# Performance work log

Measured on AMD Instinct MI355X. Metric: run time of the kernel, lower is better.

Reference implementation:

```python
import jax, jax.numpy as jnp
import numpy as np

LEAKY = 0.5      # args.leaky
TEMP = 1.0       # args.temp
N_USER = 100000  # args.user
N_ITEM = 50000   # args.item
LATDIM = 128     # args.latdim
HYPERNUM = 128   # args.hyperNum
N_LAYERS = 2     # args.gnn_layer
N_EDGES = 1000000
BATCH = 4096


def _leaky(x):
    return jnp.maximum(LEAKY * x, x)


def _l2norm(x):
    # torch.nn.functional.normalize(p=2, dim=1): x / max(||x||, 1e-12)
    n = jnp.linalg.norm(x, axis=1, keepdims=True)
    return x / jnp.maximum(n, 1e-12)


def _spmm(rows, cols, vals, x, n_out):
    # torch.sparse.mm(adj, x) with adj given as COO (rows, cols, vals)
    return jax.ops.segment_sum(vals[:, None] * x[cols], rows, num_segments=n_out)


def _hyper_prop(lats, adj, Ws):
    # lats: [N, D], adj: [N, H] (dense hyper adjacency), Ws: [3, H, H]
    lat = _leaky(adj.T @ lats)                    # [H, D]
    for k in range(3):
        # (LeakyRelu(lat.T @ W)).T + lat == LeakyRelu(W.T @ lat) + lat
        lat = _leaky(Ws[k].T @ lat) + lat
    return _leaky(adj @ lat)                      # [N, D]


def _ssl(hyperLat, gnnLat):
    pos = jnp.exp(jnp.sum(hyperLat * gnnLat, axis=1) / TEMP)
    neg = jnp.sum(jnp.exp(gnnLat @ hyperLat.T / TEMP), axis=1)
    return jnp.sum(-jnp.log(pos / (neg + 1e-8) + 1e-8))


def setup_inputs() -> dict:
    key = jax.random.key(0)
    ks = jax.random.split(key, 12)
    # distinct ids so jnp.sort(ids) == torch.unique(ids)
    uids = jax.random.permutation(ks[0], N_USER)[:BATCH].astype(jnp.int32)
    iids = jax.random.permutation(ks[1], N_ITEM)[:BATCH].astype(jnp.int32)
    adj_rows = jax.random.randint(ks[2], (N_EDGES,), 0, N_USER, dtype=jnp.int32)
    adj_cols = jax.random.randint(ks[3], (N_EDGES,), 0, N_ITEM, dtype=jnp.int32)
    adj_vals = jax.random.uniform(ks[4], (N_EDGES,), dtype=jnp.float32)
    s_emb = 0.05
    s_hh = (2.0 / (HYPERNUM + HYPERNUM)) ** 0.5   # xavier_normal
    s_dh = (2.0 / (LATDIM + HYPERNUM)) ** 0.5
    s_dd = (2.0 / (LATDIM + LATDIM)) ** 0.5
    uEmbed0 = jax.random.normal(ks[5], (N_USER, LATDIM), jnp.float32) * s_emb
    iEmbed0 = jax.random.normal(ks[6], (N_ITEM, LATDIM), jnp.float32) * s_emb
    uhyper = jax.random.normal(ks[7], (LATDIM, HYPERNUM), jnp.float32) * s_dh
    ihyper = jax.random.normal(ks[8], (LATDIM, HYPERNUM), jnp.float32) * s_dh
    Wu = jax.random.normal(ks[9], (N_LAYERS, 3, HYPERNUM, HYPERNUM), jnp.float32) * s_hh
    Wi = jax.random.normal(ks[10], (N_LAYERS, 3, HYPERNUM, HYPERNUM), jnp.float32) * s_hh
    Wt = jax.random.normal(ks[11], (N_LAYERS, LATDIM, LATDIM), jnp.float32) * s_dd
    return {"uids": uids, "iids": iids, "adj_rows": adj_rows, "adj_cols": adj_cols,
            "adj_vals": adj_vals, "uEmbed0": uEmbed0, "iEmbed0": iEmbed0,
            "uhyper": uhyper, "ihyper": ihyper, "Wu": Wu, "Wi": Wi, "Wt": Wt}


def reference(uids, iids, adj_rows, adj_cols, adj_vals, uEmbed0, iEmbed0,
              uhyper, ihyper, Wu, Wi, Wt):
    # droprate = 0 => edgeDropout and feature dropout are identity
    uuHyper = uEmbed0 @ uhyper   # [N_USER, H]
    iiHyper = iEmbed0 @ ihyper   # [N_ITEM, H]
    ulats, ilats = [uEmbed0], [iEmbed0]
    gnnU, gnnI, hypU, hypI = [], [], [], []
    for l in range(N_LAYERS):
        ulat = _leaky(_spmm(adj_rows, adj_cols, adj_vals, ilats[-1], N_USER))
        ilat = _leaky(_spmm(adj_cols, adj_rows, adj_vals, ulats[-1], N_ITEM))
        hu = _hyper_prop(ulats[-1], uuHyper, Wu[l])
        hi = _hyper_prop(ilats[-1], iiHyper, Wi[l])
        gnnU.append(ulat); gnnI.append(ilat); hypU.append(hu); hypI.append(hi)
        ulats.append(ulat + hu + ulats[-1])
        ilats.append(ilat + hi + ilats[-1])
    ulat = sum(ulats)
    ilat = sum(ilats)
    preds = jnp.sum(ulat[uids] * ilat[iids], axis=-1)
    uniqU = jnp.sort(uids)  # uids are distinct -> equals torch.unique
    uniqI = jnp.sort(iids)
    ssl = jnp.asarray(0.0, jnp.float32)
    for l in range(N_LAYERS):
        ssl = ssl + _ssl(_l2norm(hypU[l][uniqU]) @ Wt[l], _l2norm(gnnU[l][uniqU]))
        ssl = ssl + _ssl(_l2norm(hypI[l][uniqI]) @ Wt[l], _l2norm(gnnI[l][uniqI]))
    reg = (jnp.sum(jnp.square(uEmbed0)) + jnp.sum(jnp.square(iEmbed0)) +
           jnp.sum(jnp.square(uhyper)) + jnp.sum(jnp.square(ihyper)))
    return preds, ssl, reg
```

## Files before the change

kernel.cpp:

```cpp
#include <hip/hip_runtime.h>

#define NU 100000
#define NI 50000
#define DD 128
#define HH 128
#define NE 1000000
#define NB 4096
#define SCHUNK 2048
#define ATBB 512

__device__ __forceinline__ float lk(float x) { return fmaxf(0.5f * x, x); }

__global__ __launch_bounds__(256) void hist_kernel(const int* __restrict__ idx,
                                                   int* __restrict__ deg, int n) {
  int e = blockIdx.x * 256 + threadIdx.x;
  if (e < n) atomicAdd(&deg[idx[e]], 1);
}

__global__ __launch_bounds__(256) void scan_bsum(const int* __restrict__ deg,
                                                 int* __restrict__ bsum, int N) {
  int b = blockIdx.x, t = threadIdx.x;
  int base = b * SCHUNK;
  int s = 0;
  for (int i = t; i < SCHUNK; i += 256) {
    int g = base + i;
    if (g < N) s += deg[g];
  }
#pragma unroll
  for (int o = 32; o > 0; o >>= 1) s += __shfl_down(s, o);
  __shared__ int ws[4];
  if ((t & 63) == 0) ws[t >> 6] = s;
  __syncthreads();
  if (t == 0) bsum[b] = ws[0] + ws[1] + ws[2] + ws[3];
}

__global__ __launch_bounds__(256) void scan_top(int* __restrict__ bsum, int G) {
  int t = threadIdx.x;
  __shared__ int sh[256];
  int v = (t < G) ? bsum[t] : 0;
  sh[t] = v;
  __syncthreads();
  for (int o = 1; o < 256; o <<= 1) {
    int add = (t >= o) ? sh[t - o] : 0;
    __syncthreads();
    sh[t] += add;
    __syncthreads();
  }
  if (t < G) bsum[t] = sh[t] - v;
}

__global__ __launch_bounds__(256) void scan_write(const int* __restrict__ deg,
                                                  const int* __restrict__ bsumx,
                                                  int* __restrict__ rowptr,
                                                  int* __restrict__ cursor,
                                                  int N, int total) {
  int b = blockIdx.x, t = threadIdx.x;
  int base = b * SCHUNK + t * 8;
  int v[8], s = 0;
#pragma unroll
  for (int i = 0; i < 8; i++) {
    int g = base + i;
    v[i] = (g < N) ? deg[g] : 0;
    s += v[i];
  }
  __shared__ int sh[256];
  sh[t] = s;
  __syncthreads();
  for (int o = 1; o < 256; o <<= 1) {
    int add = (t >= o) ? sh[t - o] : 0;
    __syncthreads();
    sh[t] += add;
    __syncthreads();
  }
  int off = bsumx[b] + sh[t] - s;
#pragma unroll
  for (int i = 0; i < 8; i++) {
    int g = base + i;
    if (g < N) { rowptr[g] = off; cursor[g] = off; }
    off += v[i];
  }
  if (b == 0 && t == 0) rowptr[N] = total;
}

__global__ __launch_bounds__(256) void scatter_kernel(const int* __restrict__ idx,
                                                      const int* __restrict__ other,
                                                      const float* __restrict__ vals,
                                                      int* __restrict__ cursor,
                                                      int* __restrict__ scol,
                                                      float* __restrict__ sval, int n) {
  int e = blockIdx.x * 256 + threadIdx.x;
  if (e < n) {
    int p = atomicAdd(&cursor[idx[e]], 1);
    scol[p] = other[e];
    sval[p] = vals[e];
  }
}

__global__ __launch_bounds__(256) void spmm_csr_kernel(
    const int* __restrict__ rowptr, const int* __restrict__ scol,
    const float* __restrict__ sval, const float* __restrict__ x,
    float* __restrict__ y, int N) {
  int w = (blockIdx.x * 256 + threadIdx.x) >> 6;
  if (w >= N) return;
  int lane = threadIdx.x & 63;
  int half = lane >> 5, l32 = lane & 31;
  const float4* x4 = (const float4*)x;
  int j0 = rowptr[w], j1 = rowptr[w + 1];
  float ax = 0.f, ay = 0.f, az = 0.f, aw = 0.f;
  int j = j0 + half;
  for (; j + 2 < j1; j += 4) {
    int c0 = scol[j], c1 = scol[j + 2];
    float v0 = sval[j], v1 = sval[j + 2];
    float4 x0 = x4[(size_t)c0 * 32 + l32];
    float4 x1 = x4[(size_t)c1 * 32 + l32];
    ax += v0 * x0.x + v1 * x1.x;
    ay += v0 * x0.y + v1 * x1.y;
    az += v0 * x0.z + v1 * x1.z;
    aw += v0 * x0.w + v1 * x1.w;
  }
  for (; j < j1; j += 2) {
    int c0 = scol[j];
    float v0 = sval[j];
    float4 x0 = x4[(size_t)c0 * 32 + l32];
    ax += v0 * x0.x; ay += v0 * x0.y; az += v0 * x0.z; aw += v0 * x0.w;
  }
  ax += __shfl_xor(ax, 32); ay += __shfl_xor(ay, 32);
  az += __shfl_xor(az, 32); aw += __shfl_xor(aw, 32);
  if (half == 0) {
    float4 r; r.x = ax; r.y = ay; r.z = az; r.w = aw;
    ((float4*)y)[(size_t)w * 32 + l32] = r;
  }
}

__global__ __launch_bounds__(256) void atb_kernel(
    const float* __restrict__ E, const float* __restrict__ X,
    float* __restrict__ part, int N) {
  __shared__ __align__(16) float Es[64][132];
  __shared__ __align__(16) float Xs[64][132];
  int t = threadIdx.x;
  int ip = (t >> 4) << 2;
  int jp = (t & 15) << 2;
  int rpb = (N + (int)gridDim.x - 1) / (int)gridDim.x;
  int n0 = blockIdx.x * rpb;
  int n1 = min(n0 + rpb, N);
  float acc[2][2][4][4] = {};
  const float4* E4 = (const float4*)E;
  const float4* X4 = (const float4*)X;
  for (int n = n0; n < n1; n += 64) {
    int nr = min(64, n1 - n);
    __syncthreads();
#pragma unroll
    for (int q = 0; q < 8; q++) {
      int f = t + (q << 8);
      int row = f >> 5, c4 = f & 31;
      float4 ev = {0.f, 0.f, 0.f, 0.f}, xv = {0.f, 0.f, 0.f, 0.f};
      if (row < nr) {
        size_t gi = (size_t)(n + row) * 32 + c4;
        ev = E4[gi]; xv = X4[gi];
      }
      *(float4*)&Es[row][c4 << 2] = ev;
      *(float4*)&Xs[row][c4 << 2] = xv;
    }
    __syncthreads();
#pragma unroll 2
    for (int rr = 0; rr < 64; rr++) {
      float4 e0 = *(const float4*)&Es[rr][ip];
      float4 e1 = *(const float4*)&Es[rr][ip + 64];
      float4 x0 = *(const float4*)&Xs[rr][jp];
      float4 x1 = *(const float4*)&Xs[rr][jp + 64];
      const float* e0p = (const float*)&e0;
      const float* e1p = (const float*)&e1;
      const float* x0p = (const float*)&x0;
      const float* x1p = (const float*)&x1;
#pragma unroll
      for (int ai = 0; ai < 4; ai++)
#pragma unroll
        for (int aj = 0; aj < 4; aj++) {
          acc[0][0][ai][aj] += e0p[ai] * x0p[aj];
          acc[0][1][ai][aj] += e0p[ai] * x1p[aj];
          acc[1][0][ai][aj] += e1p[ai] * x0p[aj];
          acc[1][1][ai][aj] += e1p[ai] * x1p[aj];
        }
    }
  }
  float* dst = part + (size_t)blockIdx.x * 16384;
#pragma unroll
  for (int rh = 0; rh < 2; rh++)
#pragma unroll
    for (int ai = 0; ai < 4; ai++) {
      int row = rh * 64 + ip + ai;
#pragma unroll
      for (int ch = 0; ch < 2; ch++) {
        float4 v;
        v.x = acc[rh][ch][ai][0]; v.y = acc[rh][ch][ai][1];
        v.z = acc[rh][ch][ai][2]; v.w = acc[rh][ch][ai][3];
        *(float4*)&dst[row * 128 + ch * 64 + jp] = v;
      }
    }
}

__global__ __launch_bounds__(256) void reduce_atb_kernel(
    const float* __restrict__ part, float* __restrict__ A) {
  int e4 = blockIdx.x * 256 + threadIdx.x;
  const float4* p4 = (const float4*)part;
  float4 s = {0.f, 0.f, 0.f, 0.f};
#pragma unroll 4
  for (int b = 0; b < ATBB; b++) {
    float4 v = p4[(size_t)b * 4096 + e4];
    s.x += v.x; s.y += v.y; s.z += v.z; s.w += v.w;
  }
  ((float4*)A)[e4] = s;
}

__global__ __launch_bounds__(256) void chain_kernel(
    const float* __restrict__ A_u, const float* __restrict__ A_i,
    const float* __restrict__ uhy, const float* __restrict__ ihy,
    const float* __restrict__ Wu_l, const float* __restrict__ Wi_l,
    float* __restrict__ B_u, float* __restrict__ B_i) {
  __shared__ float Wb[128 * 132];
  __shared__ float LA[128][16];
  __shared__ float LB[128][16];
  int side = blockIdx.x >> 3, strip = blockIdx.x & 7;
  const float* A = side ? A_i : A_u;
  const float* hy = side ? ihy : uhy;
  const float* W = side ? Wi_l : Wu_l;
  float* Bo = side ? B_i : B_u;
  int t = threadIdx.x;
  int j0 = strip * 16;
  for (int i = t; i < 2048; i += 256) LA[i >> 4][i & 15] = A[(i >> 4) * 128 + j0 + (i & 15)];
  for (int i = t; i < 16384; i += 256) Wb[(i >> 7) * 132 + (i & 127)] = hy[i];
  __syncthreads();
  int jc = t & 15, i0 = (t >> 4) * 8;
  {
    float acc[8] = {};
    for (int k = 0; k < 128; k++) {
      float lv = LA[k][jc];
      const float* wr = &Wb[k * 132 + i0];
#pragma unroll
      for (int a = 0; a < 8; a++) acc[a] += wr[a] * lv;
    }
#pragma unroll
    for (int a = 0; a < 8; a++) LB[i0 + a][jc] = lk(acc[a]);
  }
  __syncthreads();
  float (*pin)[16] = LB;
  float (*pout)[16] = LA;
  for (int s = 0; s < 3; s++) {
    for (int i = t; i < 16384; i += 256) Wb[(i >> 7) * 132 + (i & 127)] = W[s * 16384 + i];
    __syncthreads();
    float acc[8] = {};
    for (int k = 0; k < 128; k++) {
      float lv = pin[k][jc];
      const float* wr = &Wb[k * 132 + i0];
#pragma unroll
      for (int a = 0; a < 8; a++) acc[a] += wr[a] * lv;
    }
#pragma unroll
    for (int a = 0; a < 8; a++) pout[i0 + a][jc] = lk(acc[a]) + pin[i0 + a][jc];
    __syncthreads();
    float (*tmp)[16] = pin; pin = pout; pout = tmp;
  }
  for (int i = t; i < 16384; i += 256) Wb[(i >> 7) * 132 + (i & 127)] = hy[i];
  __syncthreads();
  {
    int i = t >> 1, jb = (t & 1) * 8;
    float acc[8] = {};
    for (int k = 0; k < 128; k++) {
      float hv = Wb[i * 132 + k];
      const float* lr = &pin[k][jb];
#pragma unroll
      for (int b = 0; b < 8; b++) acc[b] += hv * lr[b];
    }
#pragma unroll
    for (int b = 0; b < 8; b++) Bo[i * 128 + j0 + jb + b] = acc[b];
  }
}

__global__ __launch_bounds__(256) void nmul_upd_kernel(
    const float* __restrict__ E, const float* __restrict__ Bm,
    const float* __restrict__ gnn, float* __restrict__ cur, int N) {
  __shared__ __align__(16) float Bs[128][132];
  __shared__ __align__(16) float Es[128][132];
  int t = threadIdx.x;
  int rg = t >> 4, dg = t & 15;
  for (int k = t; k < 16384; k += 256) Bs[k >> 7][k & 127] = Bm[k];
  int ntiles = (N + 127) >> 7;
  for (int tile = blockIdx.x; tile < ntiles; tile += gridDim.x) {
    int n0 = tile << 7;
    int nr = min(128, N - n0);
    __syncthreads();
    for (int k = t; k < 16384; k += 256) {
      int rr = k >> 7, cc = k & 127;
      Es[rr][cc] = (rr < nr) ? E[(size_t)(n0 + rr) * DD + cc] : 0.f;
    }
    __syncthreads();
    float acc[8][8] = {};
    for (int h4 = 0; h4 < 128; h4 += 4) {
      float4 ev[8];
#pragma unroll
      for (int a = 0; a < 8; a++) ev[a] = *(const float4*)&Es[rg + (a << 4)][h4];
#pragma unroll
      for (int hh = 0; hh < 4; hh++) {
        float4 b0 = *(const float4*)&Bs[h4 + hh][dg << 2];
        float4 b1 = *(const float4*)&Bs[h4 + hh][(dg << 2) + 64];
#pragma unroll
        for (int a = 0; a < 8; a++) {
          float e = ((const float*)&ev[a])[hh];
          acc[a][0] += e * b0.x; acc[a][1] += e * b0.y;
          acc[a][2] += e * b0.z; acc[a][3] += e * b0.w;
          acc[a][4] += e * b1.x; acc[a][5] += e * b1.y;
          acc[a][6] += e * b1.z; acc[a][7] += e * b1.w;
        }
      }
    }
#pragma unroll
    for (int a = 0; a < 8; a++) {
      int n = n0 + rg + (a << 4);
      if (n < N) {
        size_t base = (size_t)n * DD + (dg << 2);
        float4 g0 = *(const float4*)(gnn + base);
        float4 g1 = *(const float4*)(gnn + base + 64);
        float4 c0 = *(const float4*)(cur + base);
        float4 c1 = *(const float4*)(cur + base + 64);
        c0.x += lk(g0.x) + lk(acc[a][0]); c0.y += lk(g0.y) + lk(acc[a][1]);
        c0.z += lk(g0.z) + lk(acc[a][2]); c0.w += lk(g0.w) + lk(acc[a][3]);
        c1.x += lk(g1.x) + lk(acc[a][4]); c1.y += lk(g1.y) + lk(acc[a][5]);
        c1.z += lk(g1.z) + lk(acc[a][6]); c1.w += lk(g1.w) + lk(acc[a][7]);
        *(float4*)(cur + base) = c0; *(float4*)(cur + base + 64) = c1;
      }
    }
  }
}

__global__ __launch_bounds__(128) void sslgath_kernel(
    const int* __restrict__ ids, const float* __restrict__ gnn,
    const float* __restrict__ E, const float* __restrict__ Bm,
    float* __restrict__ og, float* __restrict__ oh) {
  __shared__ __align__(16) float Bs[128][132];
  __shared__ __align__(16) float Eb[32][132];
  __shared__ int idb[32];
  int t = threadIdx.x;
  int base = blockIdx.x * 32;
  if (t < 32) idb[t] = ids[base + t];
#pragma unroll
  for (int q = 0; q < 32; q++) {
    int f = t + q * 128;
    *(float4*)&Bs[f >> 5][(f & 31) << 2] = ((const float4*)Bm)[f];
  }
  __syncthreads();
#pragma unroll
  for (int q = 0; q < 8; q++) {
    int f = t + q * 128;
    int r = f >> 5, c4 = f & 31;
    *(float4*)&Eb[r][c4 << 2] = ((const float4*)E)[(size_t)idb[r] * 32 + c4];
  }
  __syncthreads();
  float acc[32] = {};
  for (int k = 0; k < 128; k++) {
    float b = Bs[k][t];
#pragma unroll
    for (int r = 0; r < 32; r++) acc[r] += Eb[r][k] * b;
  }
  for (int r = 0; r < 32; r++) {
    int id = idb[r];
    og[(size_t)(base + r) * DD + t] = lk(gnn[(size_t)id * DD + t]);
    oh[(size_t)(base + r) * DD + t] = lk(acc[r]);
  }
}

__global__ __launch_bounds__(128) void gaccum_kernel(
    const int* __restrict__ ids, const float* __restrict__ cur,
    float* __restrict__ sumg) {
  int b = blockIdx.x, d = threadIdx.x;
  int id = ids[b];
  sumg[(size_t)b * DD + d] += cur[(size_t)id * DD + d];
}

__global__ __launch_bounds__(256) void preds_kernel(
    const float* __restrict__ su, const float* __restrict__ si,
    float* __restrict__ outp) {
  int gid = blockIdx.x * 256 + threadIdx.x;
  int w = gid >> 6, lane = gid & 63;
  if (w >= NB) return;
  float2 a = *(const float2*)(su + (size_t)w * DD + 2 * lane);
  float2 b = *(const float2*)(si + (size_t)w * DD + 2 * lane);
  float d = a.x * b.x + a.y * b.y;
#pragma unroll
  for (int o = 32; o > 0; o >>= 1) d += __shfl_down(d, o);
  if (lane == 0) outp[w] = d;
}

__global__ __launch_bounds__(256) void sumsq_kernel(
    const float* __restrict__ x, int n, float* __restrict__ outp) {
  float acc = 0.f;
  for (int i = blockIdx.x * 256 + threadIdx.x; i < n; i += gridDim.x * 256) {
    float v = x[i];
    acc += v * v;
  }
#pragma unroll
  for (int o = 32; o > 0; o >>= 1) acc += __shfl_down(acc, o);
  __shared__ float s[4];
  if ((threadIdx.x & 63) == 0) s[threadIdx.x >> 6] = acc;
  __syncthreads();
  if (threadIdx.x == 0) atomicAdd(outp, s[0] + s[1] + s[2] + s[3]);
}

__global__ __launch_bounds__(128) void norm_kernel(
    const float* __restrict__ gh, float* __restrict__ gg,
    float* __restrict__ hn) {
  int r = blockIdx.x, d = threadIdx.x;
  __shared__ float red[4];
  float hv = gh[(size_t)r * DD + d];
  float gv = gg[(size_t)r * DD + d];
  float h2 = hv * hv, g2 = gv * gv;
#pragma unroll
  for (int o = 32; o > 0; o >>= 1) { h2 += __shfl_down(h2, o); g2 += __shfl_down(g2, o); }
  if ((d & 63) == 0) { red[(d >> 6) * 2] = h2; red[(d >> 6) * 2 + 1] = g2; }
  __syncthreads();
  float hnorm = sqrtf(red[0] + red[2]);
  float gnorm = sqrtf(red[1] + red[3]);
  hn[(size_t)r * DD + d] = hv / fmaxf(hnorm, 1e-12f);
  gg[(size_t)r * DD + d] = gv / fmaxf(gnorm, 1e-12f);
}

__global__ __launch_bounds__(256) void nmul_plain_kernel(
    const float* __restrict__ In, const float* __restrict__ Wm,
    float* __restrict__ outp) {
  __shared__ __align__(16) float Bs[128][132];
  __shared__ __align__(16) float Es[128][132];
  int t = threadIdx.x;
  int rg = t >> 4, dg = t & 15;
  int n0 = blockIdx.x << 7;
  for (int k = t; k < 16384; k += 256) {
    Bs[k >> 7][k & 127] = Wm[k];
    Es[k >> 7][k & 127] = In[(size_t)n0 * DD + k];
  }
  __syncthreads();
  float acc[8][8] = {};
  for (int h4 = 0; h4 < 128; h4 += 4) {
    float4 ev[8];
#pragma unroll
    for (int a = 0; a < 8; a++) ev[a] = *(const float4*)&Es[rg + (a << 4)][h4];
#pragma unroll
    for (int hh = 0; hh < 4; hh++) {
      float4 b0 = *(const float4*)&Bs[h4 + hh][dg << 2];
      float4 b1 = *(const float4*)&Bs[h4 + hh][(dg << 2) + 64];
#pragma unroll
      for (int a = 0; a < 8; a++) {
        float e = ((const float*)&ev[a])[hh];
        acc[a][0] += e * b0.x; acc[a][1] += e * b0.y;
        acc[a][2] += e * b0.z; acc[a][3] += e * b0.w;
        acc[a][4] += e * b1.x; acc[a][5] += e * b1.y;
        acc[a][6] += e * b1.z; acc[a][7] += e * b1.w;
      }
    }
  }
#pragma unroll
  for (int a = 0; a < 8; a++) {
    size_t base = (size_t)(n0 + rg + (a << 4)) * DD + (dg << 2);
    float4 v0, v1;
    v0.x = acc[a][0]; v0.y = acc[a][1]; v0.z = acc[a][2]; v0.w = acc[a][3];
    v1.x = acc[a][4]; v1.y = acc[a][5]; v1.z = acc[a][6]; v1.w = acc[a][7];
    *(float4*)(outp + base) = v0;
    *(float4*)(outp + base + 64) = v1;
  }
}

__global__ __launch_bounds__(256) void gram_kernel(
    const float* __restrict__ gn, const float* __restrict__ hw,
    float* __restrict__ neg) {
  __shared__ __align__(16) float Gs[128][132];
  __shared__ __align__(16) float Ht[128][132];
  int t = threadIdx.x;
  int rg = t >> 4, jp = (t & 15) << 2;
  int i0 = blockIdx.x << 7, j0 = blockIdx.y << 7;
  for (int k = t; k < 16384; k += 256) {
    int rr = k >> 7, cc = k & 127;
    Gs[rr][cc] = gn[(size_t)(i0 + rr) * DD + cc];
    Ht[cc][rr] = hw[(size_t)(j0 + rr) * DD + cc];
  }
  __syncthreads();
  float acc[8][8] = {};
  for (int h4 = 0; h4 < 128; h4 += 4) {
    float4 ev[8];
#pragma unroll
    for (int a = 0; a < 8; a++) ev[a] = *(const float4*)&Gs[rg + (a << 4)][h4];
#pragma unroll
    for (int hh = 0; hh < 4; hh++) {
      float4 b0 = *(const float4*)&Ht[h4 + hh][jp];
      float4 b1 = *(const float4*)&Ht[h4 + hh][jp + 64];
#pragma unroll
      for (int a = 0; a < 8; a++) {
        float g = ((const float*)&ev[a])[hh];
        acc[a][0] += g * b0.x; acc[a][1] += g * b0.y;
        acc[a][2] += g * b0.z; acc[a][3] += g * b0.w;
        acc[a][4] += g * b1.x; acc[a][5] += g * b1.y;
        acc[a][6] += g * b1.z; acc[a][7] += g * b1.w;
      }
    }
  }
#pragma unroll
  for (int a = 0; a < 8; a++) {
    float s = 0.f;
#pragma unroll
    for (int b = 0; b < 8; b++) s += expf(acc[a][b]);
    s += __shfl_xor(s, 1);
    s += __shfl_xor(s, 2);
    s += __shfl_xor(s, 4);
    s += __shfl_xor(s, 8);
    if ((t & 15) == 0) atomicAdd(&neg[i0 + rg + (a << 4)], s);
  }
}

__global__ __launch_bounds__(256) void sslfin_kernel(
    const float* __restrict__ gn, const float* __restrict__ hw,
    const float* __restrict__ neg, float* __restrict__ outp) {
  int gid = blockIdx.x * 256 + threadIdx.x;
  int w = gid >> 6, lane = gid & 63;
  if (w >= NB) return;
  float2 a = *(const float2*)(gn + (size_t)w * DD + 2 * lane);
  float2 b = *(const float2*)(hw + (size_t)w * DD + 2 * lane);
  float d = a.x * b.x + a.y * b.y;
#pragma unroll
  for (int o = 32; o > 0; o >>= 1) d += __shfl_down(d, o);
  if (lane == 0) {
    float pos = expf(d);
    float v = -logf(pos / (neg[w] + 1e-8f) + 1e-8f);
    atomicAdd(outp, v);
  }
}

extern "C" void kernel_launch(void* const* d_in, const int* in_sizes, int n_in,
                              void* d_out, int out_size, void* d_ws, size_t ws_size,
                              hipStream_t stream) {
  (void)in_sizes; (void)n_in; (void)out_size; (void)ws_size;
  const int* uids = (const int*)d_in[0];
  const int* iids = (const int*)d_in[1];
  const int* arow = (const int*)d_in[2];
  const int* acol = (const int*)d_in[3];
  const float* avals = (const float*)d_in[4];
  const float* uE = (const float*)d_in[5];
  const float* iE = (const float*)d_in[6];
  const float* uhy = (const float*)d_in[7];
  const float* ihy = (const float*)d_in[8];
  const float* Wu = (const float*)d_in[9];
  const float* Wi = (const float*)d_in[10];
  const float* Wt = (const float*)d_in[11];
  float* out = (float*)d_out;

  float* p = (float*)d_ws;
  float* cur_u = p; p += (size_t)NU * DD;
  float* gnn_u = p; p += (size_t)NU * DD;
  float* cur_i = p; p += (size_t)NI * DD;
  float* gnn_i = p; p += (size_t)NI * DD;
  float* A_u = p; p += HH * DD;
  float* A_i = p; p += HH * DD;
  float* B_u = p; p += HH * DD;
  float* B_i = p; p += HH * DD;
  float* sumg_u = p; p += (size_t)NB * DD;
  float* sumg_i = p; p += (size_t)NB * DD;
  float* region = p; p += (size_t)ATBB * 16384;
  float* negb = p; p += 4 * NB;
  int* rowptr_u = (int*)p; p += NU + 1;
  int* cursor_u = (int*)p; p += NU;
  int* rowptr_i = (int*)p; p += NI + 1;
  int* cursor_i = (int*)p; p += NI;
  int* bsum = (int*)p; p += 256;
  int* scol_u = (int*)p; p += NE;
  float* sval_u = p; p += NE;
  int* scol_i = (int*)p; p += NE;
  float* sval_i = p; p += NE;

  float* Apart = region;
  float* gg = region;
  float* gh = region + (size_t)NB * DD;
  float* hn = region + 2 * (size_t)NB * DD;

  const int GU = (NU + SCHUNK - 1) / SCHUNK;
  const int GI = (NI + SCHUNK - 1) / SCHUNK;
  const int EB = (NE + 255) / 256;

  hipMemsetAsync(cursor_u, 0, NU * sizeof(int), stream);
  hist_kernel<<<EB, 256, 0, stream>>>(arow, cursor_u, NE);
  scan_bsum<<<GU, 256, 0, stream>>>(cursor_u, bsum, NU);
  scan_top<<<1, 256, 0, stream>>>(bsum, GU);
  scan_write<<<GU, 256, 0, stream>>>(cursor_u, bsum, rowptr_u, cursor_u, NU, NE);
  scatter_kernel<<<EB, 256, 0, stream>>>(arow, acol, avals, cursor_u, scol_u, sval_u, NE);

  hipMemsetAsync(cursor_i, 0, NI * sizeof(int), stream);
  hist_kernel<<<EB, 256, 0, stream>>>(acol, cursor_i, NE);
  scan_bsum<<<GI, 256, 0, stream>>>(cursor_i, bsum, NI);
  scan_top<<<1, 256, 0, stream>>>(bsum, GI);
  scan_write<<<GI, 256, 0, stream>>>(cursor_i, bsum, rowptr_i, cursor_i, NI, NE);
  scatter_kernel<<<EB, 256, 0, stream>>>(acol, arow, avals, cursor_i, scol_i, sval_i, NE);

  hipMemcpyAsync(cur_u, uE, (size_t)NU * DD * 4, hipMemcpyDeviceToDevice, stream);
  hipMemcpyAsync(cur_i, iE, (size_t)NI * DD * 4, hipMemcpyDeviceToDevice, stream);
  hipMemsetAsync(out + NB, 0, 2 * sizeof(float), stream);
  hipMemsetAsync(negb, 0, 4 * NB * sizeof(float), stream);
  hipMemsetAsync(sumg_u, 0, 2 * (size_t)NB * DD * 4, stream);
  gaccum_kernel<<<NB, 128, 0, stream>>>(uids, uE, sumg_u);
  gaccum_kernel<<<NB, 128, 0, stream>>>(iids, iE, sumg_i);

  for (int l = 0; l < 2; l++) {
    const float* Wt_l = Wt + (size_t)l * DD * DD;
    spmm_csr_kernel<<<NU / 4, 256, 0, stream>>>(rowptr_u, scol_u, sval_u, cur_i, gnn_u, NU);
    spmm_csr_kernel<<<NI / 4, 256, 0, stream>>>(rowptr_i, scol_i, sval_i, cur_u, gnn_i, NI);
    atb_kernel<<<ATBB, 256, 0, stream>>>(uE, cur_u, Apart, NU);
    reduce_atb_kernel<<<16, 256, 0, stream>>>(Apart, A_u);
    atb_kernel<<<ATBB, 256, 0, stream>>>(iE, cur_i, Apart, NI);
    reduce_atb_kernel<<<16, 256, 0, stream>>>(Apart, A_i);
    chain_kernel<<<16, 256, 0, stream>>>(A_u, A_i, uhy, ihy,
        Wu + (size_t)l * 3 * HH * HH, Wi + (size_t)l * 3 * HH * HH, B_u, B_i);

    sslgath_kernel<<<NB / 32, 128, 0, stream>>>(uids, gnn_u, uE, B_u, gg, gh);
    nmul_upd_kernel<<<512, 256, 0, stream>>>(uE, B_u, gnn_u, cur_u, NU);
    gaccum_kernel<<<NB, 128, 0, stream>>>(uids, cur_u, sumg_u);
    norm_kernel<<<NB, 128, 0, stream>>>(gh, gg, hn);
    nmul_plain_kernel<<<NB / 128, 256, 0, stream>>>(hn, Wt_l, gh);
    gram_kernel<<<dim3(NB / 128, NB / 128), 256, 0, stream>>>(gg, gh, negb + (2 * l) * NB);
    sslfin_kernel<<<NB / 4, 256, 0, stream>>>(gg, gh, negb + (2 * l) * NB, out + NB);

    sslgath_kernel<<<NB / 32, 128, 0, stream>>>(iids, gnn_i, iE, B_i, gg, gh);
    nmul_upd_kernel<<<512, 256, 0, stream>>>(iE, B_i, gnn_i, cur_i, NI);
    gaccum_kernel<<<NB, 128, 0, stream>>>(iids, cur_i, sumg_i);
    norm_kernel<<<NB, 128, 0, stream>>>(gh, gg, hn);
    nmul_plain_kernel<<<NB / 128, 256, 0, stream>>>(hn, Wt_l, gh);
    gram_kernel<<<dim3(NB / 128, NB / 128), 256, 0, stream>>>(gg, gh, negb + (2 * l + 1) * NB);
    sslfin_kernel<<<NB / 4, 256, 0, stream>>>(gg, gh, negb + (2 * l + 1) * NB, out + NB);
  }

  preds_kernel<<<NB / 4, 256, 0, stream>>>(sumg_u, sumg_i, out);
  sumsq_kernel<<<2048, 256, 0, stream>>>(uE, NU * DD, out + NB + 1);
  sumsq_kernel<<<1024, 256, 0, stream>>>(iE, NI * DD, out + NB + 1);
  sumsq_kernel<<<64, 256, 0, stream>>>(uhy, DD * HH, out + NB + 1);
  sumsq_kernel<<<64, 256, 0, stream>>>(ihy, DD * HH, out + NB + 1);
}
```

Measured before the change: 2.390 ms.

## Restructure dense GEMM kernels to stream activations from global and shrink LDS tiles

Three dense matmul kernels (node update, Wt projection, SSL gram) stop staging the activation tile in shared memory. Each thread now reads its rows straight from global memory as float4 and keeps only the 128x128 (or 64x128, XOR-swizzled) weight tile in LDS. Tiles are smaller and grids larger (one 128-row tile per block with 512 threads, 32-row blocks, 64-column gram tiles), which raises occupancy and parallelism for the small 4096-row SSL matrices. The cost is repeated global or L2 reads of activations across the thread groups that share a row, and lower register-level reuse per thread.

```diff
diff --git a/kernel.cpp b/kernel.cpp
--- a/kernel.cpp
+++ b/kernel.cpp
@@ -276,58 +276,59 @@
   }
 }
 
-__global__ __launch_bounds__(256) void nmul_upd_kernel(
+__global__ __launch_bounds__(512) void nmul_upd_kernel(
     const float* __restrict__ E, const float* __restrict__ Bm,
     const float* __restrict__ gnn, float* __restrict__ cur, int N) {
-  __shared__ __align__(16) float Bs[128][132];
-  __shared__ __align__(16) float Es[128][132];
+  __shared__ __align__(16) float Bs[128][128];
   int t = threadIdx.x;
-  int rg = t >> 4, dg = t & 15;
-  for (int k = t; k < 16384; k += 256) Bs[k >> 7][k & 127] = Bm[k];
-  int ntiles = (N + 127) >> 7;
-  for (int tile = blockIdx.x; tile < ntiles; tile += gridDim.x) {
-    int n0 = tile << 7;
-    int nr = min(128, N - n0);
-    __syncthreads();
-    for (int k = t; k < 16384; k += 256) {
-      int rr = k >> 7, cc = k & 127;
-      Es[rr][cc] = (rr < nr) ? E[(size_t)(n0 + rr) * DD + cc] : 0.f;
-    }
-    __syncthreads();
-    float acc[8][8] = {};
-    for (int h4 = 0; h4 < 128; h4 += 4) {
-      float4 ev[8];
-#pragma unroll
-      for (int a = 0; a < 8; a++) ev[a] = *(const float4*)&Es[rg + (a << 4)][h4];
-#pragma unroll
-      for (int hh = 0; hh < 4; hh++) {
-        float4 b0 = *(const float4*)&Bs[h4 + hh][dg << 2];
-        float4 b1 = *(const float4*)&Bs[h4 + hh][(dg << 2) + 64];
-#pragma unroll
-        for (int a = 0; a < 8; a++) {
-          float e = ((const float*)&ev[a])[hh];
-          acc[a][0] += e * b0.x; acc[a][1] += e * b0.y;
-          acc[a][2] += e * b0.z; acc[a][3] += e * b0.w;
-          acc[a][4] += e * b1.x; acc[a][5] += e * b1.y;
-          acc[a][6] += e * b1.z; acc[a][7] += e * b1.w;
-        }
+  int dg = t & 15, rg = t >> 4;
+  const float4* B4 = (const float4*)Bm;
+#pragma unroll
+  for (int q = 0; q < 8; q++) {
+    int f = t + (q << 9);
+    *(float4*)&Bs[f >> 5][(f & 31) << 2] = B4[f];
+  }
+  __syncthreads();
+  int n0 = blockIdx.x << 7;
+  const float4* E4 = (const float4*)E;
+  float acc[4][8] = {};
+  int rows[4];
+  bool val[4];
+#pragma unroll
+  for (int a = 0; a < 4; a++) { rows[a] = n0 + rg + (a << 5); val[a] = rows[a] < N; }
+  for (int h4 = 0; h4 < 128; h4 += 4) {
+    float4 ev[4];
+#pragma unroll
+    for (int a = 0; a < 4; a++)
+      ev[a] = val[a] ? E4[(size_t)rows[a] * 32 + (h4 >> 2)]
+                     : make_float4(0.f, 0.f, 0.f, 0.f);
+#pragma unroll
+    for (int hh = 0; hh < 4; hh++) {
+      float4 b0 = *(const float4*)&Bs[h4 + hh][dg << 2];
+      float4 b1 = *(const float4*)&Bs[h4 + hh][(dg << 2) + 64];
+#pragma unroll
+      for (int a = 0; a < 4; a++) {
+        float e = ((const float*)&ev[a])[hh];
+        acc[a][0] += e * b0.x; acc[a][1] += e * b0.y;
+        acc[a][2] += e * b0.z; acc[a][3] += e * b0.w;
+        acc[a][4] += e * b1.x; acc[a][5] += e * b1.y;
+        acc[a][6] += e * b1.z; acc[a][7] += e * b1.w;
       }
     }
-#pragma unroll
-    for (int a = 0; a < 8; a++) {
-      int n = n0 + rg + (a << 4);
-      if (n < N) {
-        size_t base = (size_t)n * DD + (dg << 2);
-        float4 g0 = *(const float4*)(gnn + base);
-        float4 g1 = *(const float4*)(gnn + base + 64);
-        float4 c0 = *(const float4*)(cur + base);
-        float4 c1 = *(const float4*)(cur + base + 64);
-        c0.x += lk(g0.x) + lk(acc[a][0]); c0.y += lk(g0.y) + lk(acc[a][1]);
-        c0.z += lk(g0.z) + lk(acc[a][2]); c0.w += lk(g0.w) + lk(acc[a][3]);
-        c1.x += lk(g1.x) + lk(acc[a][4]); c1.y += lk(g1.y) + lk(acc[a][5]);
-        c1.z += lk(g1.z) + lk(acc[a][6]); c1.w += lk(g1.w) + lk(acc[a][7]);
-        *(float4*)(cur + base) = c0; *(float4*)(cur + base + 64) = c1;
-      }
+  }
+#pragma unroll
+  for (int a = 0; a < 4; a++) {
+    if (val[a]) {
+      size_t base = (size_t)rows[a] * DD + (dg << 2);
+      float4 g0 = *(const float4*)(gnn + base);
+      float4 g1 = *(const float4*)(gnn + base + 64);
+      float4 c0 = *(const float4*)(cur + base);
+      float4 c1 = *(const float4*)(cur + base + 64);
+      c0.x += lk(g0.x) + lk(acc[a][0]); c0.y += lk(g0.y) + lk(acc[a][1]);
+      c0.z += lk(g0.z) + lk(acc[a][2]); c0.w += lk(g0.w) + lk(acc[a][3]);
+      c1.x += lk(g1.x) + lk(acc[a][4]); c1.y += lk(g1.y) + lk(acc[a][5]);
+      c1.z += lk(g1.z) + lk(acc[a][6]); c1.w += lk(g1.w) + lk(acc[a][7]);
+      *(float4*)(cur + base) = c0; *(float4*)(cur + base + 64) = c1;
     }
   }
 }
@@ -426,27 +427,30 @@
 __global__ __launch_bounds__(256) void nmul_plain_kernel(
     const float* __restrict__ In, const float* __restrict__ Wm,
     float* __restrict__ outp) {
-  __shared__ __align__(16) float Bs[128][132];
-  __shared__ __align__(16) float Es[128][132];
+  __shared__ __align__(16) float Bs[128][128];
   int t = threadIdx.x;
-  int rg = t >> 4, dg = t & 15;
-  int n0 = blockIdx.x << 7;
-  for (int k = t; k < 16384; k += 256) {
-    Bs[k >> 7][k & 127] = Wm[k];
-    Es[k >> 7][k & 127] = In[(size_t)n0 * DD + k];
-  }
-  __syncthreads();
-  float acc[8][8] = {};
+  int dg = t & 15, rg = t >> 4;
+  const float4* W4 = (const float4*)Wm;
+#pragma unroll
+  for (int q = 0; q < 16; q++) {
+    int f = t + (q << 8);
+    *(float4*)&Bs[f >> 5][(f & 31) << 2] = W4[f];
+  }
+  __syncthreads();
+  int n0 = blockIdx.x << 5;
+  const float4* I4 = (const float4*)In;
+  float acc[2][8] = {};
   for (int h4 = 0; h4 < 128; h4 += 4) {
-    float4 ev[8];
-#pragma unroll
-    for (int a = 0; a < 8; a++) ev[a] = *(const float4*)&Es[rg + (a << 4)][h4];
+    float4 ev[2];
+#pragma unroll
+    for (int a = 0; a < 2; a++)
+      ev[a] = I4[(size_t)(n0 + rg + (a << 4)) * 32 + (h4 >> 2)];
 #pragma unroll
     for (int hh = 0; hh < 4; hh++) {
       float4 b0 = *(const float4*)&Bs[h4 + hh][dg << 2];
       float4 b1 = *(const float4*)&Bs[h4 + hh][(dg << 2) + 64];
 #pragma unroll
-      for (int a = 0; a < 8; a++) {
+      for (int a = 0; a < 2; a++) {
         float e = ((const float*)&ev[a])[hh];
         acc[a][0] += e * b0.x; acc[a][1] += e * b0.y;
         acc[a][2] += e * b0.z; acc[a][3] += e * b0.w;
@@ -456,7 +460,7 @@
     }
   }
 #pragma unroll
-  for (int a = 0; a < 8; a++) {
+  for (int a = 0; a < 2; a++) {
     size_t base = (size_t)(n0 + rg + (a << 4)) * DD + (dg << 2);
     float4 v0, v1;
     v0.x = acc[a][0]; v0.y = acc[a][1]; v0.z = acc[a][2]; v0.w = acc[a][3];
@@ -469,46 +473,48 @@
 __global__ __launch_bounds__(256) void gram_kernel(
     const float* __restrict__ gn, const float* __restrict__ hw,
     float* __restrict__ neg) {
-  __shared__ __align__(16) float Gs[128][132];
-  __shared__ __align__(16) float Ht[128][132];
+  __shared__ __align__(16) float Hs[64][128];
   int t = threadIdx.x;
-  int rg = t >> 4, jp = (t & 15) << 2;
-  int i0 = blockIdx.x << 7, j0 = blockIdx.y << 7;
-  for (int k = t; k < 16384; k += 256) {
-    int rr = k >> 7, cc = k & 127;
-    Gs[rr][cc] = gn[(size_t)(i0 + rr) * DD + cc];
-    Ht[cc][rr] = hw[(size_t)(j0 + rr) * DD + cc];
-  }
-  __syncthreads();
-  float acc[8][8] = {};
+  int rg = t >> 4, dg = t & 15;
+  int i0 = blockIdx.x << 7, j0 = blockIdx.y << 6;
+  float4* Hs4 = (float4*)Hs;
+  const float4* hw4 = (const float4*)hw;
+#pragma unroll
+  for (int q = 0; q < 8; q++) {
+    int f = t + (q << 8);
+    int j = f >> 5, k4 = f & 31;
+    Hs4[j * 32 + (k4 ^ ((j >> 2) & 7))] = hw4[(size_t)(j0 + j) * 32 + k4];
+  }
+  __syncthreads();
+  const float4* G4 = (const float4*)gn;
+  float acc[8][4] = {};
   for (int h4 = 0; h4 < 128; h4 += 4) {
-    float4 ev[8];
-#pragma unroll
-    for (int a = 0; a < 8; a++) ev[a] = *(const float4*)&Gs[rg + (a << 4)][h4];
-#pragma unroll
-    for (int hh = 0; hh < 4; hh++) {
-      float4 b0 = *(const float4*)&Ht[h4 + hh][jp];
-      float4 b1 = *(const float4*)&Ht[h4 + hh][jp + 64];
-#pragma unroll
-      for (int a = 0; a < 8; a++) {
-        float g = ((const float*)&ev[a])[hh];
-        acc[a][0] += g * b0.x; acc[a][1] += g * b0.y;
-        acc[a][2] += g * b0.z; acc[a][3] += g * b0.w;
-        acc[a][4] += g * b1.x; acc[a][5] += g * b1.y;
-        acc[a][6] += g * b1.z; acc[a][7] += g * b1.w;
-      }
-    }
+    int k4 = h4 >> 2;
+    float4 gv[8];
+#pragma unroll
+    for (int a = 0; a < 8; a++)
+      gv[a] = G4[(size_t)(i0 + rg + (a << 4)) * 32 + k4];
+    float4 bv[4];
+#pragma unroll
+    for (int jj = 0; jj < 4; jj++) {
+      int j = (dg << 2) + jj;
+      bv[jj] = *(const float4*)&Hs[j][(k4 ^ ((j >> 2) & 7)) << 2];
+    }
+#pragma unroll
+    for (int a = 0; a < 8; a++)
+#pragma unroll
+      for (int jj = 0; jj < 4; jj++)
+        acc[a][jj] += gv[a].x * bv[jj].x + gv[a].y * bv[jj].y +
+                      gv[a].z * bv[jj].z + gv[a].w * bv[jj].w;
   }
 #pragma unroll
   for (int a = 0; a < 8; a++) {
-    float s = 0.f;
-#pragma unroll
-    for (int b = 0; b < 8; b++) s += expf(acc[a][b]);
+    float s = expf(acc[a][0]) + expf(acc[a][1]) + expf(acc[a][2]) + expf(acc[a][3]);
     s += __shfl_xor(s, 1);
     s += __shfl_xor(s, 2);
     s += __shfl_xor(s, 4);
     s += __shfl_xor(s, 8);
-    if ((t & 15) == 0) atomicAdd(&neg[i0 + rg + (a << 4)], s);
+    if (dg == 0) atomicAdd(&neg[i0 + rg + (a << 4)], s);
   }
 }
 
@@ -579,6 +585,8 @@
   const int GU = (NU + SCHUNK - 1) / SCHUNK;
   const int GI = (NI + SCHUNK - 1) / SCHUNK;
   const int EB = (NE + 255) / 256;
+  const int TU = (NU + 127) >> 7;
+  const int TI = (NI + 127) >> 7;
 
   hipMemsetAsync(cursor_u, 0, NU * sizeof(int), stream);
   hist_kernel<<<EB, 256, 0, stream>>>(arow, cursor_u, NE);
@@ -614,19 +622,19 @@
         Wu + (size_t)l * 3 * HH * HH, Wi + (size_t)l * 3 * HH * HH, B_u, B_i);
 
     sslgath_kernel<<<NB / 32, 128, 0, stream>>>(uids, gnn_u, uE, B_u, gg, gh);
-    nmul_upd_kernel<<<512, 256, 0, stream>>>(uE, B_u, gnn_u, cur_u, NU);
+    nmul_upd_kernel<<<TU, 512, 0, stream>>>(uE, B_u, gnn_u, cur_u, NU);
     gaccum_kernel<<<NB, 128, 0, stream>>>(uids, cur_u, sumg_u);
     norm_kernel<<<NB, 128, 0, stream>>>(gh, gg, hn);
-    nmul_plain_kernel<<<NB / 128, 256, 0, stream>>>(hn, Wt_l, gh);
-    gram_kernel<<<dim3(NB / 128, NB / 128), 256, 0, stream>>>(gg, gh, negb + (2 * l) * NB);
+    nmul_plain_kernel<<<NB / 32, 256, 0, stream>>>(hn, Wt_l, gh);
+    gram_kernel<<<dim3(NB / 128, NB / 64), 256, 0, stream>>>(gg, gh, negb + (2 * l) * NB);
     sslfin_kernel<<<NB / 4, 256, 0, stream>>>(gg, gh, negb + (2 * l) * NB, out + NB);
 
     sslgath_kernel<<<NB / 32, 128, 0, stream>>>(iids, gnn_i, iE, B_i, gg, gh);
-    nmul_upd_kernel<<<512, 256, 0, stream>>>(iE, B_i, gnn_i, cur_i, NI);
+    nmul_upd_kernel<<<TI, 512, 0, stream>>>(iE, B_i, gnn_i, cur_i, NI);
     gaccum_kernel<<<NB, 128, 0, stream>>>(iids, cur_i, sumg_i);
     norm_kernel<<<NB, 128, 0, stream>>>(gh, gg, hn);
-    nmul_plain_kernel<<<NB / 128, 256, 0, stream>>>(hn, Wt_l, gh);
-    gram_kernel<<<dim3(NB / 128, NB / 128), 256, 0, stream>>>(gg, gh, negb + (2 * l + 1) * NB);
+    nmul_plain_kernel<<<NB / 32, 256, 0, stream>>>(hn, Wt_l, gh);
+    gram_kernel<<<dim3(NB / 128, NB / 64), 256, 0, stream>>>(gg, gh, negb + (2 * l + 1) * NB);
     sslfin_kernel<<<NB / 4, 256, 0, stream>>>(gg, gh, negb + (2 * l + 1) * NB, out + NB);
   }
 
```

Result: faster. 2.217 ms (-7.2%).
